# Kernel tuning notes

Measured on AMD Instinct MI355X. Metric: run time of the kernel, lower is better.

Reference implementation:

```python
import jax, jax.numpy as jnp
import numpy as np

ENTITY_TOTAL = 100000
RELATION_TOTAL = 500
NUM_RELATIONS = 2 * RELATION_TOTAL  # 1000
DIM = 128
NUM_BASES = 4
NUM_EDGES = 600000


def setup_inputs() -> dict:
    key = jax.random.key(0)
    ks = jax.random.split(key, 16)
    d = {}
    d['entity'] = jnp.arange(ENTITY_TOTAL, dtype=jnp.int64 if jax.config.jax_enable_x64 else jnp.int32)
    d['edge_index'] = jax.random.randint(ks[0], (2, NUM_EDGES), 0, ENTITY_TOTAL)
    d['edge_type'] = jax.random.randint(ks[1], (NUM_EDGES,), 0, NUM_RELATIONS)
    d['edge_norm'] = jax.random.uniform(ks[2], (NUM_EDGES,), dtype=jnp.float32)
    d['DAD_rel'] = jax.random.normal(ks[3], (RELATION_TOTAL, RELATION_TOTAL), dtype=jnp.float32)
    # learned parameters
    d['entity_table'] = jax.random.normal(ks[4], (ENTITY_TOTAL, DIM), dtype=jnp.float32)
    d['relation_emb'] = jax.random.normal(ks[5], (RELATION_TOTAL, DIM), dtype=jnp.float32) * (6.0 / (RELATION_TOTAL + DIM)) ** 0.5
    def rgcn_params(k):
        k1, k2, k3 = jax.random.split(k, 3)
        basis = jax.random.normal(k1, (NUM_BASES, DIM, DIM), dtype=jnp.float32) / np.sqrt(DIM)
        att = jax.random.normal(k2, (NUM_RELATIONS, NUM_BASES), dtype=jnp.float32) / np.sqrt(NUM_BASES)
        root = jax.random.normal(k3, (DIM, DIM), dtype=jnp.float32) / np.sqrt(DIM)
        bias = jnp.zeros((DIM,), dtype=jnp.float32)
        return basis, att, root, bias
    d['basis1'], d['att1'], d['root1'], d['bias1'] = rgcn_params(ks[6])
    d['basis2'], d['att2'], d['root2'], d['bias2'] = rgcn_params(ks[7])
    return d


def rgcn_conv(x, edge_index, edge_type, edge_norm, basis, att, root, bias):
    # PyG-style basis-decomposed RGCNConv, aggr='mean', source_to_target flow.
    num_nodes = x.shape[0]
    src, dst = edge_index[0], edge_index[1]
    x_j = x[src]                     # [E, in] gather
    att_e = att[edge_type]           # [E, B]
    # per-edge relation transform: sum_b att_e[:,b] * (x_j @ basis[b]); loop over
    # NUM_BASES (=4) avoids materializing [E, in, out].
    msg = jnp.zeros((x_j.shape[0], basis.shape[2]), dtype=x.dtype)
    for b in range(basis.shape[0]):
        msg = msg + att_e[:, b:b + 1] * (x_j @ basis[b])
    msg = msg * edge_norm[:, None]
    agg = jax.ops.segment_sum(msg, dst, num_segments=num_nodes)
    deg = jax.ops.segment_sum(jnp.ones_like(edge_norm), dst, num_segments=num_nodes)
    agg = agg / jnp.maximum(deg, 1.0)[:, None]   # mean aggregation
    return agg + x @ root + bias


def reference(entity, edge_index, edge_type, edge_norm, DAD_rel,
              entity_table, relation_emb,
              basis1, att1, root1, bias1,
              basis2, att2, root2, bias2):
    h = entity_table[entity]  # embedding lookup [N, dim]
    h = jax.nn.relu(rgcn_conv(h, edge_index, edge_type, edge_norm, basis1, att1, root1, bias1))
    # dropout(p=0.2) is identity in eval mode (deterministic reference)
    h = rgcn_conv(h, edge_index, edge_type, edge_norm, basis2, att2, root2, bias2)
    return (h, relation_emb)
```

## Files before the change

### kernel.cpp

```cpp
#include <hip/hip_runtime.h>
#include <hip/hip_bf16.h>

#define NROWS 100000
#define EDGES 600000
#define DIM 128
#define SCAN_B 391

typedef unsigned short u16;
typedef __attribute__((ext_vector_type(8))) short v8s;
typedef __attribute__((ext_vector_type(4))) float v4f;

static __device__ __forceinline__ float bf2f(u16 u) {
  union { unsigned u; float f; } c;
  c.u = (unsigned)u << 16;
  return c.f;
}
static __device__ __forceinline__ u16 f2bf(float f) {
  union { float f; unsigned u; } c;
  c.f = f;
  unsigned r = c.u + 0x7fff + ((c.u >> 16) & 1);
  return (u16)(r >> 16);
}
static __device__ __forceinline__ long ld_idx(const void* p, long i, int is64) {
  return is64 ? (long)((const long long*)p)[i] : (long)((const int*)p)[i];
}
static __device__ __forceinline__ float ld_f(const int* flags, const void* p, long i) {
  return flags[0] ? ((const float*)p)[i] : bf2f(((const u16*)p)[i]);
}

__global__ __launch_bounds__(256) void detect_kernel(
    const u16* __restrict__ table, const void* __restrict__ entity,
    const void* __restrict__ ei, const void* __restrict__ et,
    int* __restrict__ flags) {
  int gid = blockIdx.x * 256 + threadIdx.x;
  const ushort4* t4 = (const ushort4*)table;
  ushort4 v = t4[gid];
  int cf = ((((v.x >> 7) & 0xFF) == 0xFF) ? 1 : 0) +
           ((((v.y >> 7) & 0xFF) == 0xFF) ? 1 : 0) +
           ((((v.z >> 7) & 0xFF) == 0xFF) ? 1 : 0) +
           ((((v.w >> 7) & 0xFF) == 0xFF) ? 1 : 0);
  int cei = 0, cet = 0;
  if (gid < 1024) {
    cei = (((const int*)ei)[2 * gid + 1] != 0) ? 1 : 0;
    cet = (((const int*)et)[2 * gid + 1] != 0) ? 1 : 0;
  }
  __shared__ int s_f, s_ei, s_et;
  if (threadIdx.x == 0) { s_f = 0; s_ei = 0; s_et = 0; }
  __syncthreads();
  if (cf) atomicAdd(&s_f, cf);
  if (cei) atomicAdd(&s_ei, cei);
  if (cet) atomicAdd(&s_et, cet);
  __syncthreads();
  if (threadIdx.x == 0) {
    if (s_f) atomicAdd(flags + 0, s_f);
    if (s_ei) atomicAdd(flags + 2, s_ei);
    if (s_et) atomicAdd(flags + 3, s_et);
  }
  if (gid == 0) flags[1] = (((const int*)entity)[1] == 0) ? 1 : 0;
}

__global__ __launch_bounds__(256) void prep_kernel(
    const int* __restrict__ flags,
    const void* __restrict__ basis0, const void* __restrict__ root0, u16* __restrict__ Wt0,
    const void* __restrict__ basis1, const void* __restrict__ root1, u16* __restrict__ Wt1,
    const void* __restrict__ att0, const void* __restrict__ att1,
    float* __restrict__ attf0, float* __restrict__ attf1,
    const void* __restrict__ bias0, const void* __restrict__ bias1,
    float* __restrict__ biasf0, float* __restrict__ biasf1,
    const void* __restrict__ rel, float* __restrict__ relout) {
  int i = blockIdx.x * 256 + threadIdx.x;
  if (i < 2 * 81920) {
    const void* basis = (i < 81920) ? basis0 : basis1;
    const void* root = (i < 81920) ? root0 : root1;
    u16* Wt = (i < 81920) ? Wt0 : Wt1;
    int j = (i < 81920) ? i : i - 81920;
    int n = j >> 7, k = j & 127;
    float v;
    if (n < 512) {
      int b = n >> 7, c = n & 127;
      v = ld_f(flags, basis, (long)b * DIM * DIM + (long)k * DIM + c);
    } else {
      v = ld_f(flags, root, (long)k * DIM + (n - 512));
    }
    Wt[j] = f2bf(v);
    return;
  }
  i -= 163840;
  if (i < 64000) { relout[i] = ld_f(flags, rel, i); return; }
  i -= 64000;
  if (i < 4000) { attf0[i] = ld_f(flags, att0, i); return; }
  i -= 4000;
  if (i < 4000) { attf1[i] = ld_f(flags, att1, i); return; }
  i -= 4000;
  if (i < 128) { biasf0[i] = ld_f(flags, bias0, i); return; }
  i -= 128;
  if (i < 128) biasf1[i] = ld_f(flags, bias1, i);
}
#define PREP_THREADS (163840 + 64000 + 4000 + 4000 + 128 + 128)

__global__ __launch_bounds__(256) void gather_kernel(const int* __restrict__ flags,
                                                     const void* __restrict__ entity,
                                                     const void* __restrict__ table,
                                                     u16* __restrict__ hbf) {
  int gid = blockIdx.x * 256 + threadIdx.x;
  int row = gid >> 5, c4 = (gid & 31) * 4;
  if (row >= NROWS) return;
  long src = ld_idx(entity, row, flags[1]);
  ushort4 o;
  if (flags[0]) {
    float4 a = *(const float4*)((const float*)table + src * DIM + c4);
    o = make_ushort4(f2bf(a.x), f2bf(a.y), f2bf(a.z), f2bf(a.w));
  } else {
    o = *(const ushort4*)((const u16*)table + src * DIM + c4);
  }
  *(ushort4*)(hbf + (long)row * DIM + c4) = o;
}

__global__ __launch_bounds__(256) void hist_kernel(const int* __restrict__ flags,
                                                   const void* __restrict__ ei,
                                                   int* __restrict__ cnt) {
  int e = blockIdx.x * 256 + threadIdx.x;
  if (e < EDGES) atomicAdd(cnt + ld_idx(ei, EDGES + e, flags[2] == 0), 1);
}

__global__ __launch_bounds__(256) void scan1_kernel(const int* __restrict__ cnt,
                                                    int* __restrict__ rowPtr,
                                                    int* __restrict__ bsum) {
  __shared__ int sh[256];
  int i = blockIdx.x * 256 + threadIdx.x;
  int v = (i < NROWS) ? cnt[i] : 0;
  sh[threadIdx.x] = v;
  __syncthreads();
#pragma unroll
  for (int off = 1; off < 256; off <<= 1) {
    int t = (threadIdx.x >= off) ? sh[threadIdx.x - off] : 0;
    __syncthreads();
    sh[threadIdx.x] += t;
    __syncthreads();
  }
  if (i < NROWS) rowPtr[i] = sh[threadIdx.x] - v;
  if (threadIdx.x == 255) bsum[blockIdx.x] = sh[255];
}

__global__ __launch_bounds__(512) void scan2_kernel(int* __restrict__ bsum,
                                                    int* __restrict__ bofs,
                                                    int* __restrict__ rowPtr) {
  __shared__ int sh[512];
  int v = (threadIdx.x < SCAN_B) ? bsum[threadIdx.x] : 0;
  sh[threadIdx.x] = v;
  __syncthreads();
#pragma unroll
  for (int off = 1; off < 512; off <<= 1) {
    int t = (threadIdx.x >= off) ? sh[threadIdx.x - off] : 0;
    __syncthreads();
    sh[threadIdx.x] += t;
    __syncthreads();
  }
  if (threadIdx.x < SCAN_B) bofs[threadIdx.x] = sh[threadIdx.x] - v;
  if (threadIdx.x == 511) rowPtr[NROWS] = sh[511];
}

__global__ __launch_bounds__(256) void scan3_kernel(int* __restrict__ rowPtr,
                                                    const int* __restrict__ bofs,
                                                    int* __restrict__ cursor) {
  int i = blockIdx.x * 256 + threadIdx.x;
  if (i >= NROWS) return;
  int r = rowPtr[i] + bofs[blockIdx.x];
  rowPtr[i] = r;
  cursor[i] = r;
}

__global__ __launch_bounds__(256) void scatter_kernel(const int* __restrict__ flags,
                                                      const void* __restrict__ ei,
                                                      const void* __restrict__ et,
                                                      const void* __restrict__ enorm,
                                                      int* __restrict__ cursor,
                                                      int* __restrict__ csr_packed,
                                                      float* __restrict__ csr_norm) {
  int e = blockIdx.x * 256 + threadIdx.x;
  if (e >= EDGES) return;
  int is64e = (flags[2] == 0), is64t = (flags[3] == 0);
  int dst = (int)ld_idx(ei, EDGES + e, is64e);
  int src = (int)ld_idx(ei, e, is64e);
  int t = (int)ld_idx(et, e, is64t);
  int pos = atomicAdd(cursor + dst, 1);
  csr_packed[pos] = src | (t << 17);
  csr_norm[pos] = ld_f(flags, enorm, e);
}

__global__ __launch_bounds__(256) void zagg_kernel(
    const int* __restrict__ rowPtr, const int* __restrict__ csr_packed,
    const float* __restrict__ csr_norm, const float* __restrict__ att_f,
    const u16* __restrict__ hin, u16* __restrict__ Z, int c0, int c1) {
  int wid = (blockIdx.x * 256 + threadIdx.x) >> 6;
  int node = c0 + wid;
  if (node >= c1) return;
  int lane = threadIdx.x & 63, d = lane * 2;
  int beg = rowPtr[node], end = rowPtr[node + 1];
  float z00 = 0.f, z01 = 0.f, z10 = 0.f, z11 = 0.f;
  float z20 = 0.f, z21 = 0.f, z30 = 0.f, z31 = 0.f;
  int pk = 0; float nrm = 0.f;
  if (beg < end) { pk = csr_packed[beg]; nrm = csr_norm[beg]; }
  for (int e = beg; e < end; ++e) {
    int pkc = pk; float nc = nrm;
    if (e + 1 < end) { pk = csr_packed[e + 1]; nrm = csr_norm[e + 1]; }
    int src = pkc & 0x1FFFF, t = pkc >> 17;
    float4 a4 = *(const float4*)(att_f + (long)t * 4);
    unsigned v = *(const unsigned*)(hin + (long)src * DIM + d);
    float x0 = bf2f((u16)(v & 0xffffu)), x1 = bf2f((u16)(v >> 16));
    float w0 = a4.x * nc, w1 = a4.y * nc, w2 = a4.z * nc, w3 = a4.w * nc;
    z00 += w0 * x0; z01 += w0 * x1;
    z10 += w1 * x0; z11 += w1 * x1;
    z20 += w2 * x0; z21 += w2 * x1;
    z30 += w3 * x0; z31 += w3 * x1;
  }
  float invd = 1.0f / fmaxf((float)(end - beg), 1.0f);
  unsigned* zp = (unsigned*)(Z + (long)(node - c0) * 512) + lane;
  zp[0]   = (unsigned)f2bf(z00 * invd) | ((unsigned)f2bf(z01 * invd) << 16);
  zp[64]  = (unsigned)f2bf(z10 * invd) | ((unsigned)f2bf(z11 * invd) << 16);
  zp[128] = (unsigned)f2bf(z20 * invd) | ((unsigned)f2bf(z21 * invd) << 16);
  zp[192] = (unsigned)f2bf(z30 * invd) | ((unsigned)f2bf(z31 * invd) << 16);
}

__global__ __launch_bounds__(256) void fgemm_kernel(
    const u16* __restrict__ Z, const u16* __restrict__ hin,
    const u16* __restrict__ Wt, const float* __restrict__ bias,
    int c0, int c1, int finalMode,
    u16* __restrict__ hout, float* __restrict__ outp) {
  __shared__ u16 Wl[128 * 136];
  int wave = threadIdx.x >> 6, lane = threadIdx.x & 63;
  int quad = lane >> 4, l16 = lane & 15;
  long lrow = (long)blockIdx.x * 64 + wave * 16 + l16;
  long arow = c0 + lrow;
  bool rv = arow < c1;

  v4f av[8];
#pragma unroll
  for (int nt = 0; nt < 8; ++nt) av[nt] = (v4f){0.f, 0.f, 0.f, 0.f};

  for (int seg = 0; seg < 5; ++seg) {
#pragma unroll
    for (int it = 0; it < 8; ++it) {
      int idx = threadIdx.x + it * 256;
      int n = idx >> 4, kk = (idx & 15) * 8;
      *(int4*)&Wl[n * 136 + kk] = *(const int4*)&Wt[(long)(seg * 128 + n) * 128 + kk];
    }
    __syncthreads();
    const u16* abase = (seg < 4) ? Z + lrow * 512 + seg * 128
                                 : hin + arow * 128;
#pragma unroll
    for (int ks = 0; ks < 4; ++ks) {
      int k0 = ks * 32;
      v8s a = {0, 0, 0, 0, 0, 0, 0, 0};
      if (rv) a = *(const v8s*)&abase[k0 + quad * 8];
#pragma unroll
      for (int nt = 0; nt < 8; ++nt) {
        v8s b = *(const v8s*)&Wl[(nt * 16 + l16) * 136 + k0 + quad * 8];
        av[nt] = __builtin_amdgcn_mfma_f32_16x16x32_bf16(a, b, av[nt], 0, 0, 0);
      }
    }
    __syncthreads();
  }

  long orow0 = c0 + (long)blockIdx.x * 64 + wave * 16 + quad * 4;
#pragma unroll
  for (int nt = 0; nt < 8; ++nt) {
    int col = nt * 16 + l16;
    float bv = bias[col];
#pragma unroll
    for (int r = 0; r < 4; ++r) {
      long row = orow0 + r;
      if (row >= c1) continue;
      float v = av[nt][r] + bv;
      if (finalMode == 1) hout[row * DIM + col] = f2bf(fmaxf(v, 0.f));
      else                outp[row * DIM + col] = v;
    }
  }
}

static size_t alignup(size_t x) { return (x + 255) & ~(size_t)255; }

extern "C" void kernel_launch(void* const* d_in, const int* in_sizes, int n_in,
                              void* d_out, int out_size, void* d_ws, size_t ws_size,
                              hipStream_t stream) {
  static const long exp_sz[15] = {100000, 1200000, 600000, 600000, 250000,
                                  12800000, 64000, 65536, 4000, 16384, 128,
                                  65536, 4000, 16384, 128};
  int map[15];
  bool posOK = (n_in >= 15);
  for (int i = 0; posOK && i < 15; ++i) posOK = (in_sizes[i] == exp_sz[i]);
  if (posOK) {
    for (int i = 0; i < 15; ++i) map[i] = i;
  } else {
    bool used[64] = {};
    for (int i = 0; i < 15; ++i) {
      map[i] = -1;
      for (int j = 0; j < n_in && j < 64; ++j)
        if (!used[j] && in_sizes[j] == exp_sz[i]) { map[i] = j; used[j] = true; break; }
      if (map[i] < 0) map[i] = (i < n_in) ? i : 0;
    }
  }
  const void* entity = d_in[map[0]];
  const void* edge_index = d_in[map[1]];
  const void* edge_type = d_in[map[2]];
  const void* edge_norm = d_in[map[3]];
  const void* table = d_in[map[5]];
  const void* rel_emb = d_in[map[6]];
  const void* basis[2] = {d_in[map[7]], d_in[map[11]]};
  const void* att[2] = {d_in[map[8]], d_in[map[12]]};
  const void* root[2] = {d_in[map[9]], d_in[map[13]]};
  const void* bias[2] = {d_in[map[10]], d_in[map[14]]};

  char* ws = (char*)d_ws;
  size_t off = 0;
  auto grab = [&](size_t bytes) { size_t o = off; off = alignup(off + bytes); return o; };
  int* flags = (int*)(ws + grab(16));
  float* att_f[2] = {(float*)(ws + grab(4000 * 4)), (float*)(ws + grab(4000 * 4))};
  float* bias_f[2] = {(float*)(ws + grab(DIM * 4)), (float*)(ws + grab(DIM * 4))};
  u16* Wt[2] = {(u16*)(ws + grab(640 * 128 * 2)), (u16*)(ws + grab(640 * 128 * 2))};
  int* cnt = (int*)(ws + grab((size_t)NROWS * 4));
  int* cursor = (int*)(ws + grab((size_t)NROWS * 4));
  int* rowPtr = (int*)(ws + grab((size_t)(NROWS + 1) * 4));
  int* bsum = (int*)(ws + grab((size_t)SCAN_B * 4));
  int* bofs = (int*)(ws + grab((size_t)SCAN_B * 4));
  int* csr_packed = (int*)(ws + grab((size_t)EDGES * 4));
  float* csr_norm = (float*)(ws + grab((size_t)EDGES * 4));
  u16* hbf = (u16*)(ws + grab((size_t)NROWS * DIM * 2));
  u16* hbf2 = (u16*)(ws + grab((size_t)NROWS * DIM * 2));
  size_t fixedB = off;

  static const int ncOrd[5] = {1, 2, 4, 8, 16};
  int NC = 16;
  for (int i = 0; i < 5; ++i) {
    int nc = ncOrd[i];
    size_t r = (NROWS + nc - 1) / nc;
    if (fixedB + alignup(r * 512 * 2) <= ws_size) { NC = nc; break; }
  }
  const int rpc = (NROWS + NC - 1) / NC;
  u16* Z = (u16*)(ws + grab((size_t)rpc * 512 * 2));

  hipMemsetAsync(flags, 0, 16, stream);
  hipMemsetAsync(cnt, 0, (size_t)NROWS * 4, stream);
  detect_kernel<<<64, 256, 0, stream>>>((const u16*)table, entity, edge_index,
                                        edge_type, flags);
  prep_kernel<<<(PREP_THREADS + 255) / 256, 256, 0, stream>>>(
      flags, basis[0], root[0], Wt[0], basis[1], root[1], Wt[1],
      att[0], att[1], att_f[0], att_f[1],
      bias[0], bias[1], bias_f[0], bias_f[1],
      rel_emb, (float*)d_out + (size_t)NROWS * DIM);
  gather_kernel<<<(NROWS * 32 + 255) / 256, 256, 0, stream>>>(flags, entity, table, hbf);
  hist_kernel<<<(EDGES + 255) / 256, 256, 0, stream>>>(flags, edge_index, cnt);
  scan1_kernel<<<SCAN_B, 256, 0, stream>>>(cnt, rowPtr, bsum);
  scan2_kernel<<<1, 512, 0, stream>>>(bsum, bofs, rowPtr);
  scan3_kernel<<<SCAN_B, 256, 0, stream>>>(rowPtr, bofs, cursor);
  scatter_kernel<<<(EDGES + 255) / 256, 256, 0, stream>>>(
      flags, edge_index, edge_type, edge_norm, cursor, csr_packed, csr_norm);

  const u16* hin = hbf;
  for (int l = 0; l < 2; ++l) {
    for (int c = 0; c < NC; ++c) {
      int c0 = c * rpc, c1 = (c0 + rpc < NROWS) ? c0 + rpc : NROWS;
      int rc = c1 - c0;
      zagg_kernel<<<(rc * 64 + 255) / 256, 256, 0, stream>>>(
          rowPtr, csr_packed, csr_norm, att_f[l], hin, Z, c0, c1);
      fgemm_kernel<<<(rc + 63) / 64, 256, 0, stream>>>(
          Z, hin, Wt[l], bias_f[l], c0, c1, (l == 0) ? 1 : 2, hbf2, (float*)d_out);
    }
    hin = hbf2;
  }
}
```

Before: 446.6 us.

## Fuse neighbor aggregation and basis GEMM into one kernel with LDS-resident Z

Replaces the separate aggregation kernel and GEMM kernel with a single 512-thread kernel. Each block aggregates 64 nodes into a shared-memory Z tile, then runs the MFMA GEMM over that tile plus the root segment. This removes the global write and re-read of the large per-node Z buffer and the chunked launch loop. The cost is about 100KB of LDS per block, which limits occupancy for the latency-bound gather phase. The aggregation and GEMM phases also no longer overlap across kernels.

```diff
diff --git a/kernel.cpp b/kernel.cpp
--- a/kernel.cpp
+++ b/kernel.cpp
@@ -188,90 +188,94 @@
   csr_norm[pos] = ld_f(flags, enorm, e);
 }
 
-__global__ __launch_bounds__(256) void zagg_kernel(
+#define ZSTRIDE 520
+__global__ __launch_bounds__(512) void azgemm_kernel(
     const int* __restrict__ rowPtr, const int* __restrict__ csr_packed,
     const float* __restrict__ csr_norm, const float* __restrict__ att_f,
-    const u16* __restrict__ hin, u16* __restrict__ Z, int c0, int c1) {
-  int wid = (blockIdx.x * 256 + threadIdx.x) >> 6;
-  int node = c0 + wid;
-  if (node >= c1) return;
-  int lane = threadIdx.x & 63, d = lane * 2;
-  int beg = rowPtr[node], end = rowPtr[node + 1];
-  float z00 = 0.f, z01 = 0.f, z10 = 0.f, z11 = 0.f;
-  float z20 = 0.f, z21 = 0.f, z30 = 0.f, z31 = 0.f;
-  int pk = 0; float nrm = 0.f;
-  if (beg < end) { pk = csr_packed[beg]; nrm = csr_norm[beg]; }
-  for (int e = beg; e < end; ++e) {
-    int pkc = pk; float nc = nrm;
-    if (e + 1 < end) { pk = csr_packed[e + 1]; nrm = csr_norm[e + 1]; }
-    int src = pkc & 0x1FFFF, t = pkc >> 17;
-    float4 a4 = *(const float4*)(att_f + (long)t * 4);
-    unsigned v = *(const unsigned*)(hin + (long)src * DIM + d);
-    float x0 = bf2f((u16)(v & 0xffffu)), x1 = bf2f((u16)(v >> 16));
-    float w0 = a4.x * nc, w1 = a4.y * nc, w2 = a4.z * nc, w3 = a4.w * nc;
-    z00 += w0 * x0; z01 += w0 * x1;
-    z10 += w1 * x0; z11 += w1 * x1;
-    z20 += w2 * x0; z21 += w2 * x1;
-    z30 += w3 * x0; z31 += w3 * x1;
-  }
-  float invd = 1.0f / fmaxf((float)(end - beg), 1.0f);
-  unsigned* zp = (unsigned*)(Z + (long)(node - c0) * 512) + lane;
-  zp[0]   = (unsigned)f2bf(z00 * invd) | ((unsigned)f2bf(z01 * invd) << 16);
-  zp[64]  = (unsigned)f2bf(z10 * invd) | ((unsigned)f2bf(z11 * invd) << 16);
-  zp[128] = (unsigned)f2bf(z20 * invd) | ((unsigned)f2bf(z21 * invd) << 16);
-  zp[192] = (unsigned)f2bf(z30 * invd) | ((unsigned)f2bf(z31 * invd) << 16);
-}
-
-__global__ __launch_bounds__(256) void fgemm_kernel(
-    const u16* __restrict__ Z, const u16* __restrict__ hin,
-    const u16* __restrict__ Wt, const float* __restrict__ bias,
-    int c0, int c1, int finalMode,
+    const u16* __restrict__ hin, const u16* __restrict__ Wt,
+    const float* __restrict__ bias, int finalMode,
     u16* __restrict__ hout, float* __restrict__ outp) {
+  __shared__ u16 Zl[64][ZSTRIDE];
   __shared__ u16 Wl[128 * 136];
-  int wave = threadIdx.x >> 6, lane = threadIdx.x & 63;
+  int wv = threadIdx.x >> 6, lane = threadIdx.x & 63;
+  int row0 = blockIdx.x * 64;
+  int d = lane * 2;
+
+  for (int i = 0; i < 8; ++i) {
+    int lr = (wv << 3) + i;
+    int node = row0 + lr;
+    int beg = 0, end = 0;
+    if (node < NROWS) { beg = rowPtr[node]; end = rowPtr[node + 1]; }
+    float z00 = 0.f, z01 = 0.f, z10 = 0.f, z11 = 0.f;
+    float z20 = 0.f, z21 = 0.f, z30 = 0.f, z31 = 0.f;
+    int pk = 0; float nrm = 0.f;
+    if (beg < end) { pk = csr_packed[beg]; nrm = csr_norm[beg]; }
+    for (int e = beg; e < end; ++e) {
+      int pkc = pk; float nc = nrm;
+      if (e + 1 < end) { pk = csr_packed[e + 1]; nrm = csr_norm[e + 1]; }
+      int src = pkc & 0x1FFFF, t = pkc >> 17;
+      float4 a4 = *(const float4*)(att_f + (long)t * 4);
+      unsigned v = *(const unsigned*)(hin + (long)src * DIM + d);
+      float x0 = bf2f((u16)(v & 0xffffu)), x1 = bf2f((u16)(v >> 16));
+      float w0 = a4.x * nc, w1 = a4.y * nc, w2 = a4.z * nc, w3 = a4.w * nc;
+      z00 += w0 * x0; z01 += w0 * x1;
+      z10 += w1 * x0; z11 += w1 * x1;
+      z20 += w2 * x0; z21 += w2 * x1;
+      z30 += w3 * x0; z31 += w3 * x1;
+    }
+    float invd = 1.0f / fmaxf((float)(end - beg), 1.0f);
+    *(unsigned*)&Zl[lr][d]       = (unsigned)f2bf(z00 * invd) | ((unsigned)f2bf(z01 * invd) << 16);
+    *(unsigned*)&Zl[lr][128 + d] = (unsigned)f2bf(z10 * invd) | ((unsigned)f2bf(z11 * invd) << 16);
+    *(unsigned*)&Zl[lr][256 + d] = (unsigned)f2bf(z20 * invd) | ((unsigned)f2bf(z21 * invd) << 16);
+    *(unsigned*)&Zl[lr][384 + d] = (unsigned)f2bf(z30 * invd) | ((unsigned)f2bf(z31 * invd) << 16);
+  }
+
+  int rt = wv >> 1, ct = wv & 1;
   int quad = lane >> 4, l16 = lane & 15;
-  long lrow = (long)blockIdx.x * 64 + wave * 16 + l16;
-  long arow = c0 + lrow;
-  bool rv = arow < c1;
-
-  v4f av[8];
-#pragma unroll
-  for (int nt = 0; nt < 8; ++nt) av[nt] = (v4f){0.f, 0.f, 0.f, 0.f};
+  v4f acc[4];
+#pragma unroll
+  for (int nt = 0; nt < 4; ++nt) acc[nt] = (v4f){0.f, 0.f, 0.f, 0.f};
+
+  long arow = row0 + rt * 16 + l16;
+  bool rv = arow < NROWS;
 
   for (int seg = 0; seg < 5; ++seg) {
-#pragma unroll
-    for (int it = 0; it < 8; ++it) {
-      int idx = threadIdx.x + it * 256;
+    __syncthreads();
+#pragma unroll
+    for (int it = 0; it < 4; ++it) {
+      int idx = threadIdx.x + it * 512;
       int n = idx >> 4, kk = (idx & 15) * 8;
       *(int4*)&Wl[n * 136 + kk] = *(const int4*)&Wt[(long)(seg * 128 + n) * 128 + kk];
     }
     __syncthreads();
-    const u16* abase = (seg < 4) ? Z + lrow * 512 + seg * 128
-                                 : hin + arow * 128;
 #pragma unroll
     for (int ks = 0; ks < 4; ++ks) {
       int k0 = ks * 32;
-      v8s a = {0, 0, 0, 0, 0, 0, 0, 0};
-      if (rv) a = *(const v8s*)&abase[k0 + quad * 8];
-#pragma unroll
-      for (int nt = 0; nt < 8; ++nt) {
-        v8s b = *(const v8s*)&Wl[(nt * 16 + l16) * 136 + k0 + quad * 8];
-        av[nt] = __builtin_amdgcn_mfma_f32_16x16x32_bf16(a, b, av[nt], 0, 0, 0);
+      v8s a;
+      if (seg < 4) {
+        a = *(const v8s*)&Zl[rt * 16 + l16][seg * 128 + k0 + quad * 8];
+      } else {
+        a = (v8s){0, 0, 0, 0, 0, 0, 0, 0};
+        if (rv) a = *(const v8s*)&hin[arow * DIM + k0 + quad * 8];
       }
-    }
-    __syncthreads();
-  }
-
-  long orow0 = c0 + (long)blockIdx.x * 64 + wave * 16 + quad * 4;
-#pragma unroll
-  for (int nt = 0; nt < 8; ++nt) {
-    int col = nt * 16 + l16;
+#pragma unroll
+      for (int nt = 0; nt < 4; ++nt) {
+        v8s b = *(const v8s*)&Wl[(ct * 64 + nt * 16 + l16) * 136 + k0 + quad * 8];
+        acc[nt] = __builtin_amdgcn_mfma_f32_16x16x32_bf16(a, b, acc[nt], 0, 0, 0);
+      }
+    }
+  }
+
+  long orow0 = row0 + rt * 16 + quad * 4;
+#pragma unroll
+  for (int nt = 0; nt < 4; ++nt) {
+    int col = ct * 64 + nt * 16 + l16;
     float bv = bias[col];
 #pragma unroll
     for (int r = 0; r < 4; ++r) {
       long row = orow0 + r;
-      if (row >= c1) continue;
-      float v = av[nt][r] + bv;
+      if (row >= NROWS) continue;
+      float v = acc[nt][r] + bv;
       if (finalMode == 1) hout[row * DIM + col] = f2bf(fmaxf(v, 0.f));
       else                outp[row * DIM + col] = v;
     }
@@ -327,17 +331,6 @@
   float* csr_norm = (float*)(ws + grab((size_t)EDGES * 4));
   u16* hbf = (u16*)(ws + grab((size_t)NROWS * DIM * 2));
   u16* hbf2 = (u16*)(ws + grab((size_t)NROWS * DIM * 2));
-  size_t fixedB = off;
-
-  static const int ncOrd[5] = {1, 2, 4, 8, 16};
-  int NC = 16;
-  for (int i = 0; i < 5; ++i) {
-    int nc = ncOrd[i];
-    size_t r = (NROWS + nc - 1) / nc;
-    if (fixedB + alignup(r * 512 * 2) <= ws_size) { NC = nc; break; }
-  }
-  const int rpc = (NROWS + NC - 1) / NC;
-  u16* Z = (u16*)(ws + grab((size_t)rpc * 512 * 2));
 
   hipMemsetAsync(flags, 0, 16, stream);
   hipMemsetAsync(cnt, 0, (size_t)NROWS * 4, stream);
@@ -356,16 +349,12 @@
   scatter_kernel<<<(EDGES + 255) / 256, 256, 0, stream>>>(
       flags, edge_index, edge_type, edge_norm, cursor, csr_packed, csr_norm);
 
+  const int blocks = (NROWS + 63) / 64;
   const u16* hin = hbf;
   for (int l = 0; l < 2; ++l) {
-    for (int c = 0; c < NC; ++c) {
-      int c0 = c * rpc, c1 = (c0 + rpc < NROWS) ? c0 + rpc : NROWS;
-      int rc = c1 - c0;
-      zagg_kernel<<<(rc * 64 + 255) / 256, 256, 0, stream>>>(
-          rowPtr, csr_packed, csr_norm, att_f[l], hin, Z, c0, c1);
-      fgemm_kernel<<<(rc + 63) / 64, 256, 0, stream>>>(
-          Z, hin, Wt[l], bias_f[l], c0, c1, (l == 0) ? 1 : 2, hbf2, (float*)d_out);
-    }
+    azgemm_kernel<<<blocks, 512, 0, stream>>>(
+        rowPtr, csr_packed, csr_norm, att_f[l], hin, Wt[l], bias_f[l],
+        (l == 0) ? 1 : 2, hbf2, (float*)d_out);
     hin = hbf2;
   }
 }
```

Result: slower. 672.3 us (+50.5%).
